# Kernel tuning notes

Hardware: AMD Instinct MI355X
Metric: run time of the kernel (lower is better)

## Reference

```python
import jax, jax.numpy as jnp
import numpy as np

N_HEADS = 8; N_LEVELS = 4; T_WINDOW = 2; N_CURR = 4; N_TEMP = 2; D_MODEL = 256
D_HEAD = D_MODEL // N_HEADS
SHAPES = [[4, 32, 48], [4, 16, 24], [4, 8, 12], [4, 4, 6]]  # (T, H, W) per level
LEN_IN = sum(t * h * w for t, h, w in SHAPES)  # 8160
LEN_Q = LEN_IN
N_BATCH = 1


def _bilinear_sample(value_l, loc):
    # value_l: (N, M, H, W, D); loc: (N, M, Q, P, 2) normalized to [0, 1].
    # Matches torch grid_sample(mode='bilinear', padding_mode='zeros', align_corners=False)
    # with grid = 2*loc - 1, i.e. pixel coords x = loc_x*W - 0.5, y = loc_y*H - 0.5.
    N, M, H, W, D = value_l.shape
    Q, P = loc.shape[2], loc.shape[3]
    x = loc[..., 0] * W - 0.5
    y = loc[..., 1] * H - 0.5
    x0 = jnp.floor(x); y0 = jnp.floor(y)
    wx = x - x0; wy = y - y0
    flat = value_l.reshape(N, M, H * W, D)

    def gather(xi, yi):
        valid = ((xi >= 0) & (xi < W) & (yi >= 0) & (yi < H)).astype(value_l.dtype)
        idx = (jnp.clip(yi, 0, H - 1) * W + jnp.clip(xi, 0, W - 1)).astype(jnp.int32)
        g = jnp.take_along_axis(flat, idx.reshape(N, M, Q * P, 1), axis=2)
        return g.reshape(N, M, Q, P, D) * valid[..., None]

    v00 = gather(x0, y0); v10 = gather(x0 + 1.0, y0)
    v01 = gather(x0, y0 + 1.0); v11 = gather(x0 + 1.0, y0 + 1.0)
    return (v00 * ((1 - wx) * (1 - wy))[..., None] + v10 * (wx * (1 - wy))[..., None]
            + v01 * ((1 - wx) * wy)[..., None] + v11 * (wx * wy)[..., None])


def _forward(query, reference_points, temporal_offsets, input_flatten, shapes, starts,
             Wv, bv, Ws, bs, Wa, ba, Wts, bts, Wta, bta, Wo, bo):
    N, Lq, _ = query.shape
    value = (input_flatten @ Wv + bv).reshape(N, -1, N_HEADS, D_HEAD)
    ts_off = (query @ Wts + bts).reshape(N, Lq, N_HEADS, N_LEVELS, T_WINDOW, N_TEMP, 2)
    t_attn = (query @ Wta + bta).reshape(N, Lq, N_HEADS, N_LEVELS * T_WINDOW * N_TEMP)
    c_attn = (query @ Wa + ba).reshape(N, Lq, N_HEADS, N_LEVELS * N_CURR)
    # joint softmax over current + temporal sampling points (as in the source)
    attn = jax.nn.softmax(jnp.concatenate([c_attn, t_attn], axis=-1), axis=-1)
    aw_c = attn[..., :N_LEVELS * N_CURR].reshape(N, Lq, N_HEADS, N_LEVELS, N_CURR)
    aw_t = attn[..., N_LEVELS * N_CURR:].reshape(N, Lq, N_HEADS, N_LEVELS, T_WINDOW * N_TEMP)
    aw = jnp.concatenate([aw_c, aw_t], axis=4)  # (N, Lq, M, L, P)
    c_off = (query @ Ws + bs).reshape(N, Lq, N_HEADS, N_LEVELS, N_CURR, 2)
    # flattened-temporal grid per level: width W_l, height T_l*H_l
    norm = jnp.array([[w, t * h] for t, h, w in shapes], dtype=query.dtype)  # (L, 2)
    loc_c = reference_points[:, :, None, :, None, :] + c_off / norm[None, None, None, :, None, :]
    loc_t = (reference_points[:, :, None, :, None, None, :]
             + temporal_offsets[:, :, None, :, :, None, :]
             + ts_off / norm[None, None, None, :, None, None, :])
    loc_t = loc_t.reshape(N, Lq, N_HEADS, N_LEVELS, T_WINDOW * N_TEMP, 2)
    locs = jnp.concatenate([loc_c, loc_t], axis=4)  # (N, Lq, M, L, P, 2)
    out = jnp.zeros((N, N_HEADS, Lq, D_HEAD), query.dtype)
    for l, (t, h, w) in enumerate(shapes):
        s = starts[l]
        vl = value[:, s:s + t * h * w].transpose(0, 2, 1, 3).reshape(N, N_HEADS, t * h, w, D_HEAD)
        loc_l = locs[:, :, :, l].transpose(0, 2, 1, 3, 4)   # (N, M, Lq, P, 2)
        sampled = _bilinear_sample(vl, loc_l)               # (N, M, Lq, P, Dh)
        w_l = aw[:, :, :, l].transpose(0, 2, 1, 3)          # (N, M, Lq, P)
        out = out + jnp.einsum('nmqpd,nmqp->nmqd', sampled, w_l)
    out = out.transpose(0, 2, 1, 3).reshape(N, Lq, D_MODEL)
    return out @ Wo + bo


def setup_inputs() -> dict:
    key = jax.random.key(0)
    ks = jax.random.split(key, 18)
    D = D_MODEL
    sc = 0.02
    query = jax.random.normal(ks[0], (N_BATCH, LEN_Q, D), jnp.float32)
    reference_points = jax.random.uniform(ks[1], (N_BATCH, LEN_Q, N_LEVELS, 2), jnp.float32)
    temporal_offsets = jax.random.uniform(ks[2], (N_BATCH, LEN_Q, N_LEVELS, T_WINDOW, 2),
                                          jnp.float32, minval=-0.25, maxval=0.25)
    input_flatten = jax.random.normal(ks[3], (N_BATCH, LEN_IN, D), jnp.float32)
    input_spatial_shapes = jnp.array(SHAPES, dtype=jnp.int32)
    starts = np.cumsum([0] + [t * h * w for t, h, w in SHAPES])[:-1]
    input_level_start_index = jnp.array(starts, dtype=jnp.int32)
    n_off = N_HEADS * N_LEVELS * N_CURR * 2          # 256
    n_att = N_HEADS * N_LEVELS * N_CURR              # 128
    n_toff = N_HEADS * N_LEVELS * T_WINDOW * N_TEMP * 2  # 256
    n_tatt = N_HEADS * N_LEVELS * T_WINDOW * N_TEMP      # 128
    return {
        'query': query, 'reference_points': reference_points,
        'temporal_offsets': temporal_offsets, 'input_flatten': input_flatten,
        'input_spatial_shapes': input_spatial_shapes,
        'input_level_start_index': input_level_start_index,
        'Wv': jax.random.normal(ks[4], (D, D), jnp.float32) * sc,
        'bv': jnp.zeros((D,), jnp.float32),
        'Ws': jax.random.normal(ks[5], (D, n_off), jnp.float32) * sc,
        'bs': jax.random.normal(ks[6], (n_off,), jnp.float32) * 2.0,
        'Wa': jax.random.normal(ks[7], (D, n_att), jnp.float32) * sc,
        'ba': jnp.zeros((n_att,), jnp.float32),
        'Wts': jax.random.normal(ks[8], (D, n_toff), jnp.float32) * sc,
        'bts': jax.random.normal(ks[9], (n_toff,), jnp.float32) * 2.0,
        'Wta': jax.random.normal(ks[10], (D, n_tatt), jnp.float32) * sc,
        'bta': jnp.zeros((n_tatt,), jnp.float32),
        'Wo': jax.random.normal(ks[11], (D, D), jnp.float32) * sc,
        'bo': jnp.zeros((D,), jnp.float32),
    }


def reference(query, reference_points, temporal_offsets, input_flatten,
              input_spatial_shapes, input_level_start_index,
              Wv, bv, Ws, bs, Wa, ba, Wts, bts, Wta, bta, Wo, bo):
    shapes = [tuple(int(v) for v in row) for row in np.asarray(input_spatial_shapes)]
    starts = [int(v) for v in np.asarray(input_level_start_index)]
    return _forward(query, reference_points, temporal_offsets, input_flatten,
                    shapes, starts, Wv, bv, Ws, bs, Wa, ba, Wts, bts, Wta, bta, Wo, bo)
```

## Files before the change

kernel.cpp:

```cpp
#include <hip/hip_runtime.h>


#define LEN 8160
#define NPACK8 (1280 * 256 / 8)

typedef __attribute__((ext_vector_type(8))) short bf16x8;
typedef __attribute__((ext_vector_type(8))) unsigned short u16x8;
typedef __attribute__((ext_vector_type(4))) float f32x4;

__device__ __forceinline__ unsigned short rne_bf16(float v)
{
    unsigned u = __float_as_uint(v);
    return (unsigned short)((u + 0x7FFFu + ((u >> 16) & 1u)) >> 16);
}

__device__ __forceinline__ void split_bf16(float v, unsigned short* hi, unsigned short* lo)
{
    unsigned u = __float_as_uint(v);
    unsigned r = (u + 0x7FFFu + ((u >> 16) & 1u)) & 0xFFFF0000u;
    float hif = __uint_as_float(r);
    float lof = v - hif;
    unsigned ul = __float_as_uint(lof);
    unsigned rl = (ul + 0x7FFFu + ((ul >> 16) & 1u)) >> 16;
    *hi = (unsigned short)(r >> 16);
    *lo = (unsigned short)rl;
}

__device__ __forceinline__ float bf2f(unsigned short s)
{
    return __uint_as_float(((unsigned)s) << 16);
}

__device__ __forceinline__ void splitA8(const float* a, bf16x8* hi, bf16x8* lo)
{
    float4 x = *(const float4*)a;
    float4 y = *(const float4*)(a + 4);
    unsigned short h[8], l[8];
    split_bf16(x.x, &h[0], &l[0]); split_bf16(x.y, &h[1], &l[1]);
    split_bf16(x.z, &h[2], &l[2]); split_bf16(x.w, &h[3], &l[3]);
    split_bf16(y.x, &h[4], &l[4]); split_bf16(y.y, &h[5], &l[5]);
    split_bf16(y.z, &h[6], &l[6]); split_bf16(y.w, &h[7], &l[7]);
    bf16x8 hv, lv;
    #pragma unroll
    for (int i = 0; i < 8; i++) { hv[i] = (short)h[i]; lv[i] = (short)l[i]; }
    *hi = hv; *lo = lv;
}

__global__ __launch_bounds__(256) void prep_kernel(
    const float* __restrict__ Ws, const float* __restrict__ bs,
    const float* __restrict__ Wa, const float* __restrict__ ba,
    const float* __restrict__ Wts, const float* __restrict__ bts,
    const float* __restrict__ Wta, const float* __restrict__ bta,
    const float* __restrict__ Wv, const float* __restrict__ Wo,
    unsigned short* __restrict__ Whi, unsigned short* __restrict__ Wlo,
    float* __restrict__ bcat)
{
    int idx = blockIdx.x * 256 + threadIdx.x;
    if (idx < NPACK8) {
        int n = idx >> 5;
        int k0 = (idx & 31) << 3;
        unsigned short h[8], l[8];
        #pragma unroll
        for (int t = 0; t < 8; t++) {
            int k = k0 + t;
            float v;
            if (n < 256) v = Wv[k * 256 + n];
            else if (n < 1024) {
                int j = n - 256;
                if (j < 256)      v = Ws [k * 256 + j];
                else if (j < 384) v = Wa [k * 128 + (j - 256)];
                else if (j < 640) v = Wts[k * 256 + (j - 384)];
                else              v = Wta[k * 128 + (j - 640)];
            } else v = Wo[k * 256 + (n - 1024)];
            split_bf16(v, &h[t], &l[t]);
        }
        uint4 hv, lv;
        hv.x = h[0] | ((unsigned)h[1] << 16); hv.y = h[2] | ((unsigned)h[3] << 16);
        hv.z = h[4] | ((unsigned)h[5] << 16); hv.w = h[6] | ((unsigned)h[7] << 16);
        lv.x = l[0] | ((unsigned)l[1] << 16); lv.y = l[2] | ((unsigned)l[3] << 16);
        lv.z = l[4] | ((unsigned)l[5] << 16); lv.w = l[6] | ((unsigned)l[7] << 16);
        *(uint4*)(Whi + n * 256 + k0) = hv;
        *(uint4*)(Wlo + n * 256 + k0) = lv;
    } else if (idx < NPACK8 + 768) {
        int j = idx - NPACK8;
        float v;
        if (j < 256)      v = bs[j];
        else if (j < 384) v = ba[j - 256];
        else if (j < 640) v = bts[j - 384];
        else              v = bta[j - 640];
        bcat[j] = v;
    }
}

__global__ __launch_bounds__(256) void gemm_mfma_dual(
    const float* __restrict__ A0,
    const unsigned short* __restrict__ B0hi, const unsigned short* __restrict__ B0lo,
    const float* __restrict__ bias0, void* __restrict__ C0, int N0, int mode0, int nbx0,
    const float* __restrict__ A1,
    const unsigned short* __restrict__ B1hi, const unsigned short* __restrict__ B1lo,
    const float* __restrict__ bias1, void* __restrict__ C1, int N1, int mode1)
{
    __shared__ unsigned short Bf[2 * 4 * 4 * 64 * 8];
    const int tid = threadIdx.x;
    const int wave = tid >> 6, lane = tid & 63;
    int bx = blockIdx.x;
    const int by = blockIdx.y;

    const float* A;
    const unsigned short *Bhi, *Blo;
    const float* bias; void* C; int N, mode;
    if (bx < nbx0) {
        A = A0; Bhi = B0hi; Blo = B0lo;
        bias = bias0; C = C0; N = N0; mode = mode0;
    } else {
        bx -= nbx0;
        A = A1; Bhi = B1hi; Blo = B1lo;
        bias = bias1; C = C1; N = N1; mode = mode1;
    }

    const int lm = lane & 15;
    const int kq = lane >> 4;
    const int m0 = by * 128 + wave * 32 + lm;
    const int ra = min(m0, LEN - 1);
    const int rb = min(m0 + 16, LEN - 1);
    const float* aP0 = A + (size_t)ra * 256 + kq * 8;
    const float* aP1 = A + (size_t)rb * 256 + kq * 8;

    f32x4 acc[2][4] = {};
    #pragma unroll
    for (int chunk = 0; chunk < 2; chunk++) {
        #pragma unroll
        for (int t = 0; t < 8; t++) {
            int f = t * 256 + tid;
            int ln = f & 63, nt = (f >> 6) & 3, kt = (f >> 8) & 3, pl = f >> 10;
            const unsigned short* src = (pl ? Blo : Bhi)
                + (size_t)(bx * 64 + nt * 16 + (ln & 15)) * 256
                + chunk * 128 + kt * 32 + (ln >> 4) * 8;
            *(uint4*)(&Bf[(size_t)f * 8]) = *(const uint4*)src;
        }
        __syncthreads();
        #pragma unroll
        for (int kt = 0; kt < 4; kt++) {
            const int ko = chunk * 128 + kt * 32;
            bf16x8 ah0, al0, ah1, al1;
            splitA8(aP0 + ko, &ah0, &al0);
            splitA8(aP1 + ko, &ah1, &al1);
            #pragma unroll
            for (int nt = 0; nt < 4; nt++) {
                const int fb = (kt * 4 + nt) * 64 + lane;
                bf16x8 bh = *(const bf16x8*)(&Bf[(size_t)fb * 8]);
                bf16x8 bl = *(const bf16x8*)(&Bf[(size_t)(fb + 1024) * 8]);
                acc[0][nt] = __builtin_amdgcn_mfma_f32_16x16x32_bf16(ah0, bh, acc[0][nt], 0, 0, 0);
                acc[0][nt] = __builtin_amdgcn_mfma_f32_16x16x32_bf16(ah0, bl, acc[0][nt], 0, 0, 0);
                acc[0][nt] = __builtin_amdgcn_mfma_f32_16x16x32_bf16(al0, bh, acc[0][nt], 0, 0, 0);
                acc[1][nt] = __builtin_amdgcn_mfma_f32_16x16x32_bf16(ah1, bh, acc[1][nt], 0, 0, 0);
                acc[1][nt] = __builtin_amdgcn_mfma_f32_16x16x32_bf16(ah1, bl, acc[1][nt], 0, 0, 0);
                acc[1][nt] = __builtin_amdgcn_mfma_f32_16x16x32_bf16(al1, bh, acc[1][nt], 0, 0, 0);
            }
        }
        __syncthreads();
    }

    const int col = bx * 64 + lm;
    #pragma unroll
    for (int sub = 0; sub < 2; sub++) {
        const int row0 = by * 128 + wave * 32 + sub * 16 + kq * 4;
        #pragma unroll
        for (int nt = 0; nt < 4; nt++) {
            int c = col + nt * 16;
            float bb = bias[c];
            #pragma unroll
            for (int r = 0; r < 4; r++) {
                int row = row0 + r;
                if (row < LEN) {
                    float v = acc[sub][nt][r] + bb;
                    if (mode) {
                        ((unsigned short*)C)[(size_t)(c >> 5) * 8192 * 32
                                             + (size_t)row * 32 + (c & 31)] = rne_bf16(v);
                    } else {
                        ((float*)C)[(size_t)row * N + c] = v;
                    }
                }
            }
        }
    }
}

__global__ __launch_bounds__(256) void sample_kernel(
    const unsigned short* __restrict__ value,
    const float* __restrict__ proj,
    const float* __restrict__ refp,
    const float* __restrict__ toff,
    float* __restrict__ attn)
{
    const int q = blockIdx.x;
    const int head = threadIdx.x >> 5;
    const int lane = threadIdx.x & 31;
    __shared__ int2   s_row[8][32];
    __shared__ float4 s_w[8][32];

    const float* p = proj + (size_t)q * 768;

    {
        const int i = lane;
        float logit, ox, oy, rx, ry;
        int l;
        if (i < 16) {
            l = i >> 2; int pt2 = i & 3;
            logit = p[256 + head * 16 + i];
            ox = p[head * 32 + l * 8 + pt2 * 2 + 0];
            oy = p[head * 32 + l * 8 + pt2 * 2 + 1];
            rx = refp[q * 8 + l * 2 + 0];
            ry = refp[q * 8 + l * 2 + 1];
        } else {
            int j = i - 16; l = j >> 2;
            int tp = j & 3, tw = tp >> 1, nt = tp & 1;
            logit = p[640 + head * 16 + j];
            ox = p[384 + head * 32 + l * 8 + tw * 4 + nt * 2 + 0];
            oy = p[384 + head * 32 + l * 8 + tw * 4 + nt * 2 + 1];
            rx = refp[q * 8 + l * 2 + 0] + toff[q * 16 + l * 4 + tw * 2 + 0];
            ry = refp[q * 8 + l * 2 + 1] + toff[q * 16 + l * 4 + tw * 2 + 1];
        }
        const int Wl = 48 >> l;
        const int Hgl = 128 >> l;
        const int st = 8192 - (8192 >> (2 * l));
        const float fW = (float)Wl, fHg = (float)Hgl;
        float x = (rx + ox / fW) * fW - 0.5f;
        float y = (ry + oy / fHg) * fHg - 0.5f;

        float mx = logit;
        #pragma unroll
        for (int off = 16; off > 0; off >>= 1)
            mx = fmaxf(mx, __shfl_xor(mx, off, 32));
        float e = expf(logit - mx);
        float s = e;
        #pragma unroll
        for (int off = 16; off > 0; off >>= 1)
            s += __shfl_xor(s, off, 32);
        float w = e / s;

        float fx = floorf(x), fy = floorf(y);
        float wx = x - fx, wy = y - fy;
        int x0 = (int)fx, y0 = (int)fy;
        int x1 = x0 + 1, y1 = y0 + 1;
        float mx0 = ((unsigned)x0 < (unsigned)Wl) ? 1.f : 0.f;
        float mx1 = ((unsigned)x1 < (unsigned)Wl) ? 1.f : 0.f;
        float my0 = ((unsigned)y0 < (unsigned)Hgl) ? 1.f : 0.f;
        float my1 = ((unsigned)y1 < (unsigned)Hgl) ? 1.f : 0.f;
        int cx0 = min(max(x0, 0), Wl - 1), cx1 = min(max(x1, 0), Wl - 1);
        int cy0 = min(max(y0, 0), Hgl - 1), cy1 = min(max(y1, 0), Hgl - 1);
        int xb = min(max(x0, 0), Wl - 2);
        float sx0 = 1.f - wx, sy0 = 1.f - wy;
        float aL = (cx0 == xb     ? sx0 * mx0 : 0.f) + (cx1 == xb     ? wx * mx1 : 0.f);
        float aR = (cx0 == xb + 1 ? sx0 * mx0 : 0.f) + (cx1 == xb + 1 ? wx * mx1 : 0.f);
        float by0 = sy0 * my0, by1 = wy * my1;
        int2 rr;
        rr.x = (st + cy0 * Wl + xb) * 64;
        rr.y = (st + cy1 * Wl + xb) * 64;
        float4 ww;
        ww.x = w * aL * by0;
        ww.y = w * aR * by0;
        ww.z = w * aL * by1;
        ww.w = w * aR * by1;
        s_row[head][lane] = rr;
        s_w[head][lane] = ww;
    }
    __syncthreads();

    const int pt4  = lane >> 3;
    const int half = (lane >> 2) & 1;
    const int cg   = lane & 3;
    const char* vbase = (const char*)value + head * (8192 * 64) + half * 64 + cg * 16;
    float acc[8] = {0.f, 0.f, 0.f, 0.f, 0.f, 0.f, 0.f, 0.f};
    #pragma unroll
    for (int i = 0; i < 8; i++) {
        int pidx = (i << 2) | pt4;
        int2 rr = s_row[head][pidx];
        float4 ww = s_w[head][pidx];
        u16x8 v0 = *(const u16x8*)(vbase + rr.x);
        u16x8 v1 = *(const u16x8*)(vbase + rr.y);
        float w0 = half ? ww.y : ww.x;
        float w1 = half ? ww.w : ww.z;
        #pragma unroll
        for (int j = 0; j < 8; j++) {
            acc[j] = fmaf(w0, bf2f(v0[j]), acc[j]);
            acc[j] = fmaf(w1, bf2f(v1[j]), acc[j]);
        }
    }
    #pragma unroll
    for (int off = 4; off <= 16; off <<= 1)
        #pragma unroll
        for (int j = 0; j < 8; j++)
            acc[j] += __shfl_xor(acc[j], off, 32);

    if (lane < 4) {
        size_t o = (size_t)q * 256 + head * 32 + cg * 8;
        *(float4*)(attn + o)     = make_float4(acc[0], acc[1], acc[2], acc[3]);
        *(float4*)(attn + o + 4) = make_float4(acc[4], acc[5], acc[6], acc[7]);
    }
}

extern "C" void kernel_launch(void* const* d_in, const int* in_sizes, int n_in,
                              void* d_out, int out_size, void* d_ws, size_t ws_size,
                              hipStream_t stream)
{
    const float* query = (const float*)d_in[0];
    const float* refp  = (const float*)d_in[1];
    const float* toff  = (const float*)d_in[2];
    const float* inpf  = (const float*)d_in[3];
    const float* Wv  = (const float*)d_in[6];
    const float* bv  = (const float*)d_in[7];
    const float* Ws_ = (const float*)d_in[8];
    const float* bs_ = (const float*)d_in[9];
    const float* Wa  = (const float*)d_in[10];
    const float* ba  = (const float*)d_in[11];
    const float* Wts = (const float*)d_in[12];
    const float* bts = (const float*)d_in[13];
    const float* Wta = (const float*)d_in[14];
    const float* bta = (const float*)d_in[15];
    const float* Wo  = (const float*)d_in[16];
    const float* bo  = (const float*)d_in[17];
    float* out = (float*)d_out;

    unsigned short* value_bf = (unsigned short*)d_ws;
    float* proj = (float*)(value_bf + (size_t)8 * 8192 * 32);
    float* attn = proj + (size_t)LEN * 768;
    unsigned short* Whi = (unsigned short*)(attn + (size_t)LEN * 256);
    unsigned short* Wlo = Whi + 1280 * 256;
    float* bcat = (float*)(Wlo + 1280 * 256);

    prep_kernel<<<164, 256, 0, stream>>>(Ws_, bs_, Wa, ba, Wts, bts, Wta, bta,
                                         Wv, Wo, Whi, Wlo, bcat);
    gemm_mfma_dual<<<dim3(16, 64), 256, 0, stream>>>(
        inpf, Whi, Wlo, bv, value_bf, 256, 1, 4,
        query, Whi + 256 * 256, Wlo + 256 * 256, bcat, proj, 768, 0);
    sample_kernel<<<LEN, 256, 0, stream>>>(value_bf, proj, refp, toff, attn);
    gemm_mfma_dual<<<dim3(4, 64), 256, 0, stream>>>(
        attn, Whi + 1024 * 256, Wlo + 1024 * 256, bo, out, 256, 0, 4,
        attn, Whi + 1024 * 256, Wlo + 1024 * 256, bo, out, 256, 0);
}
```

Before: 174.9 us.

## Pre-split attention output to bf16 hi/lo, use direct-to-LDS B loads, halve output GEMM tile

The sampling kernel now writes its result as separate bf16 hi and lo planes, so the output projection GEMM loads pre-split A operands instead of splitting fp32 on the fly. The GEMM is templated on rows per wave and A format, and the output projection runs with 64-row tiles over twice as many blocks to raise occupancy. B-tile staging switches to global_load_lds direct-to-LDS transfers with an explicit vmcnt wait. This adds split work to the sampler's epilogue and changes the LDS layout of the staged B tiles.

```diff
diff --git a/kernel.cpp b/kernel.cpp
--- a/kernel.cpp
+++ b/kernel.cpp
@@ -3,6 +3,9 @@
 
 #define LEN 8160
 #define NPACK8 (1280 * 256 / 8)
+
+#define AS1 __attribute__((address_space(1)))
+#define AS3 __attribute__((address_space(3)))
 
 typedef __attribute__((ext_vector_type(8))) short bf16x8;
 typedef __attribute__((ext_vector_type(8))) unsigned short u16x8;
@@ -92,6 +95,7 @@
     }
 }
 
+template <int MSUB, int AFMT>
 __global__ __launch_bounds__(256) void gemm_mfma_dual(
     const float* __restrict__ A0,
     const unsigned short* __restrict__ B0hi, const unsigned short* __restrict__ B0lo,
@@ -100,7 +104,7 @@
     const unsigned short* __restrict__ B1hi, const unsigned short* __restrict__ B1lo,
     const float* __restrict__ bias1, void* __restrict__ C1, int N1, int mode1)
 {
-    __shared__ unsigned short Bf[2 * 4 * 4 * 64 * 8];
+    __shared__ __align__(16) unsigned short Bf[2 * 4 * 4 * 64 * 8];
     const int tid = threadIdx.x;
     const int wave = tid >> 6, lane = tid & 63;
     int bx = blockIdx.x;
@@ -120,31 +124,59 @@
 
     const int lm = lane & 15;
     const int kq = lane >> 4;
-    const int m0 = by * 128 + wave * 32 + lm;
+    const int m0 = by * (MSUB * 64) + wave * (MSUB * 16) + lm;
     const int ra = min(m0, LEN - 1);
     const int rb = min(m0 + 16, LEN - 1);
+
     const float* aP0 = A + (size_t)ra * 256 + kq * 8;
     const float* aP1 = A + (size_t)rb * 256 + kq * 8;
-
-    f32x4 acc[2][4] = {};
+    const unsigned short* Ah = (const unsigned short*)A;
+    const unsigned short* ahP0 = Ah + (size_t)ra * 256 + kq * 8;
+    const unsigned short* alP0 = Ah + (size_t)LEN * 256 + (size_t)ra * 256 + kq * 8;
+    const unsigned short* ahP1 = Ah + (size_t)rb * 256 + kq * 8;
+    const unsigned short* alP1 = Ah + (size_t)LEN * 256 + (size_t)rb * 256 + kq * 8;
+
+    f32x4 acc[MSUB][4] = {};
     #pragma unroll
     for (int chunk = 0; chunk < 2; chunk++) {
         #pragma unroll
         for (int t = 0; t < 8; t++) {
-            int f = t * 256 + tid;
-            int ln = f & 63, nt = (f >> 6) & 3, kt = (f >> 8) & 3, pl = f >> 10;
+            const int g  = t * 4 + wave;
+            const int nt = g & 3, kt = (g >> 2) & 3, pl = g >> 4;
             const unsigned short* src = (pl ? Blo : Bhi)
-                + (size_t)(bx * 64 + nt * 16 + (ln & 15)) * 256
-                + chunk * 128 + kt * 32 + (ln >> 4) * 8;
-            *(uint4*)(&Bf[(size_t)f * 8]) = *(const uint4*)src;
-        }
+                + (size_t)(bx * 64 + nt * 16 + (lane & 15)) * 256
+                + chunk * 128 + kt * 32 + (lane >> 4) * 8;
+            __builtin_amdgcn_global_load_lds(
+                (AS1 void*)(uintptr_t)src,
+                (AS3 void*)&Bf[(size_t)g * 64 * 8],
+                16, 0, 0);
+        }
+        bf16x8 pah[MSUB][4], pal[MSUB][4];
+        if constexpr (AFMT == 1) {
+            #pragma unroll
+            for (int kt = 0; kt < 4; kt++) {
+                const int ko = chunk * 128 + kt * 32;
+                pah[0][kt] = *(const bf16x8*)(ahP0 + ko);
+                pal[0][kt] = *(const bf16x8*)(alP0 + ko);
+                if constexpr (MSUB == 2) {
+                    pah[1][kt] = *(const bf16x8*)(ahP1 + ko);
+                    pal[1][kt] = *(const bf16x8*)(alP1 + ko);
+                }
+            }
+        }
+        asm volatile("s_waitcnt vmcnt(0)" ::: "memory");
         __syncthreads();
         #pragma unroll
         for (int kt = 0; kt < 4; kt++) {
             const int ko = chunk * 128 + kt * 32;
             bf16x8 ah0, al0, ah1, al1;
-            splitA8(aP0 + ko, &ah0, &al0);
-            splitA8(aP1 + ko, &ah1, &al1);
+            if constexpr (AFMT == 0) {
+                splitA8(aP0 + ko, &ah0, &al0);
+                if constexpr (MSUB == 2) splitA8(aP1 + ko, &ah1, &al1);
+            } else {
+                ah0 = pah[0][kt]; al0 = pal[0][kt];
+                if constexpr (MSUB == 2) { ah1 = pah[1][kt]; al1 = pal[1][kt]; }
+            }
             #pragma unroll
             for (int nt = 0; nt < 4; nt++) {
                 const int fb = (kt * 4 + nt) * 64 + lane;
@@ -153,9 +185,11 @@
                 acc[0][nt] = __builtin_amdgcn_mfma_f32_16x16x32_bf16(ah0, bh, acc[0][nt], 0, 0, 0);
                 acc[0][nt] = __builtin_amdgcn_mfma_f32_16x16x32_bf16(ah0, bl, acc[0][nt], 0, 0, 0);
                 acc[0][nt] = __builtin_amdgcn_mfma_f32_16x16x32_bf16(al0, bh, acc[0][nt], 0, 0, 0);
-                acc[1][nt] = __builtin_amdgcn_mfma_f32_16x16x32_bf16(ah1, bh, acc[1][nt], 0, 0, 0);
-                acc[1][nt] = __builtin_amdgcn_mfma_f32_16x16x32_bf16(ah1, bl, acc[1][nt], 0, 0, 0);
-                acc[1][nt] = __builtin_amdgcn_mfma_f32_16x16x32_bf16(al1, bh, acc[1][nt], 0, 0, 0);
+                if constexpr (MSUB == 2) {
+                    acc[1][nt] = __builtin_amdgcn_mfma_f32_16x16x32_bf16(ah1, bh, acc[1][nt], 0, 0, 0);
+                    acc[1][nt] = __builtin_amdgcn_mfma_f32_16x16x32_bf16(ah1, bl, acc[1][nt], 0, 0, 0);
+                    acc[1][nt] = __builtin_amdgcn_mfma_f32_16x16x32_bf16(al1, bh, acc[1][nt], 0, 0, 0);
+                }
             }
         }
         __syncthreads();
@@ -163,8 +197,8 @@
 
     const int col = bx * 64 + lm;
     #pragma unroll
-    for (int sub = 0; sub < 2; sub++) {
-        const int row0 = by * 128 + wave * 32 + sub * 16 + kq * 4;
+    for (int sub = 0; sub < MSUB; sub++) {
+        const int row0 = by * (MSUB * 64) + wave * (MSUB * 16) + sub * 16 + kq * 4;
         #pragma unroll
         for (int nt = 0; nt < 4; nt++) {
             int c = col + nt * 16;
@@ -191,7 +225,7 @@
     const float* __restrict__ proj,
     const float* __restrict__ refp,
     const float* __restrict__ toff,
-    float* __restrict__ attn)
+    unsigned short* __restrict__ attn)
 {
     const int q = blockIdx.x;
     const int head = threadIdx.x >> 5;
@@ -295,8 +329,16 @@
 
     if (lane < 4) {
         size_t o = (size_t)q * 256 + head * 32 + cg * 8;
-        *(float4*)(attn + o)     = make_float4(acc[0], acc[1], acc[2], acc[3]);
-        *(float4*)(attn + o + 4) = make_float4(acc[4], acc[5], acc[6], acc[7]);
+        unsigned short h[8], l[8];
+        #pragma unroll
+        for (int j = 0; j < 8; j++) split_bf16(acc[j], &h[j], &l[j]);
+        uint4 hv, lv;
+        hv.x = h[0] | ((unsigned)h[1] << 16); hv.y = h[2] | ((unsigned)h[3] << 16);
+        hv.z = h[4] | ((unsigned)h[5] << 16); hv.w = h[6] | ((unsigned)h[7] << 16);
+        lv.x = l[0] | ((unsigned)l[1] << 16); lv.y = l[2] | ((unsigned)l[3] << 16);
+        lv.z = l[4] | ((unsigned)l[5] << 16); lv.w = l[6] | ((unsigned)l[7] << 16);
+        *(uint4*)(attn + o) = hv;
+        *(uint4*)(attn + (size_t)LEN * 256 + o) = lv;
     }
 }
 
@@ -324,18 +366,18 @@
 
     unsigned short* value_bf = (unsigned short*)d_ws;
     float* proj = (float*)(value_bf + (size_t)8 * 8192 * 32);
-    float* attn = proj + (size_t)LEN * 768;
-    unsigned short* Whi = (unsigned short*)(attn + (size_t)LEN * 256);
+    unsigned short* attn_hl = (unsigned short*)(proj + (size_t)LEN * 768);
+    unsigned short* Whi = attn_hl + (size_t)2 * LEN * 256;
     unsigned short* Wlo = Whi + 1280 * 256;
     float* bcat = (float*)(Wlo + 1280 * 256);
 
     prep_kernel<<<164, 256, 0, stream>>>(Ws_, bs_, Wa, ba, Wts, bts, Wta, bta,
                                          Wv, Wo, Whi, Wlo, bcat);
-    gemm_mfma_dual<<<dim3(16, 64), 256, 0, stream>>>(
+    gemm_mfma_dual<2, 0><<<dim3(16, 64), 256, 0, stream>>>(
         inpf, Whi, Wlo, bv, value_bf, 256, 1, 4,
         query, Whi + 256 * 256, Wlo + 256 * 256, bcat, proj, 768, 0);
-    sample_kernel<<<LEN, 256, 0, stream>>>(value_bf, proj, refp, toff, attn);
-    gemm_mfma_dual<<<dim3(4, 64), 256, 0, stream>>>(
-        attn, Whi + 1024 * 256, Wlo + 1024 * 256, bo, out, 256, 0, 4,
-        attn, Whi + 1024 * 256, Wlo + 1024 * 256, bo, out, 256, 0);
-}
+    sample_kernel<<<LEN, 256, 0, stream>>>(value_bf, proj, refp, toff, attn_hl);
+    gemm_mfma_dual<1, 1><<<dim3(4, 128), 256, 0, stream>>>(
+        (const float*)attn_hl, Whi + 1024 * 256, Wlo + 1024 * 256, bo, out, 256, 0, 4,
+        (const float*)attn_hl, Whi + 1024 * 256, Wlo + 1024 * 256, bo, out, 256, 0);
+}
```

Result: no change. 172.9 us (-1.1%).

## Fuse deformable sampling with output projection and use direct global-to-LDS loads

Applied to the files above, without the earlier changes.

The sampling kernel now handles 16 queries per 512-thread block, two teams of eight queries each. It keeps the sampled attention rows in shared memory and runs the output projection GEMM (split-bf16 MFMA) in place, so the attn buffer no longer goes through global memory and one launch is dropped. The GEMM B-tile staging now uses global_load_lds to write straight into LDS instead of going through registers. The trade-offs are a much smaller grid (510 blocks), per-query serial loops inside each team, and Wo tiles read straight from global memory by every block.

```diff
diff --git a/kernel.cpp b/kernel.cpp
--- a/kernel.cpp
+++ b/kernel.cpp
@@ -3,6 +3,9 @@
 
 #define LEN 8160
 #define NPACK8 (1280 * 256 / 8)
+
+#define AS1 __attribute__((address_space(1)))
+#define AS3 __attribute__((address_space(3)))
 
 typedef __attribute__((ext_vector_type(8))) short bf16x8;
 typedef __attribute__((ext_vector_type(8))) unsigned short u16x8;
@@ -100,7 +103,7 @@
     const unsigned short* __restrict__ B1hi, const unsigned short* __restrict__ B1lo,
     const float* __restrict__ bias1, void* __restrict__ C1, int N1, int mode1)
 {
-    __shared__ unsigned short Bf[2 * 4 * 4 * 64 * 8];
+    __shared__ __align__(16) unsigned short Bf[2 * 4 * 4 * 64 * 8];
     const int tid = threadIdx.x;
     const int wave = tid >> 6, lane = tid & 63;
     int bx = blockIdx.x;
@@ -131,13 +134,17 @@
     for (int chunk = 0; chunk < 2; chunk++) {
         #pragma unroll
         for (int t = 0; t < 8; t++) {
-            int f = t * 256 + tid;
-            int ln = f & 63, nt = (f >> 6) & 3, kt = (f >> 8) & 3, pl = f >> 10;
+            const int g  = t * 4 + wave;
+            const int nt = g & 3, kt = (g >> 2) & 3, pl = g >> 4;
             const unsigned short* src = (pl ? Blo : Bhi)
-                + (size_t)(bx * 64 + nt * 16 + (ln & 15)) * 256
-                + chunk * 128 + kt * 32 + (ln >> 4) * 8;
-            *(uint4*)(&Bf[(size_t)f * 8]) = *(const uint4*)src;
-        }
+                + (size_t)(bx * 64 + nt * 16 + (lane & 15)) * 256
+                + chunk * 128 + kt * 32 + (lane >> 4) * 8;
+            __builtin_amdgcn_global_load_lds(
+                (AS1 void*)(uintptr_t)src,
+                (AS3 void*)&Bf[(size_t)g * 64 * 8],
+                16, 0, 0);
+        }
+        asm volatile("s_waitcnt vmcnt(0)" ::: "memory");
         __syncthreads();
         #pragma unroll
         for (int kt = 0; kt < 4; kt++) {
@@ -186,117 +193,157 @@
     }
 }
 
-__global__ __launch_bounds__(256) void sample_kernel(
+__global__ __launch_bounds__(512, 4) void fused_sample_out(
     const unsigned short* __restrict__ value,
     const float* __restrict__ proj,
     const float* __restrict__ refp,
     const float* __restrict__ toff,
-    float* __restrict__ attn)
-{
-    const int q = blockIdx.x;
-    const int head = threadIdx.x >> 5;
+    const unsigned short* __restrict__ WoThi,
+    const unsigned short* __restrict__ WoTlo,
+    const float* __restrict__ bo,
+    float* __restrict__ out)
+{
+    const int team = threadIdx.x >> 8;
+    const int head = (threadIdx.x >> 5) & 7;
     const int lane = threadIdx.x & 31;
-    __shared__ int2   s_row[8][32];
-    __shared__ float4 s_w[8][32];
-
-    const float* p = proj + (size_t)q * 768;
-
-    {
-        const int i = lane;
-        float logit, ox, oy, rx, ry;
-        int l;
-        if (i < 16) {
-            l = i >> 2; int pt2 = i & 3;
-            logit = p[256 + head * 16 + i];
-            ox = p[head * 32 + l * 8 + pt2 * 2 + 0];
-            oy = p[head * 32 + l * 8 + pt2 * 2 + 1];
-            rx = refp[q * 8 + l * 2 + 0];
-            ry = refp[q * 8 + l * 2 + 1];
-        } else {
-            int j = i - 16; l = j >> 2;
-            int tp = j & 3, tw = tp >> 1, nt = tp & 1;
-            logit = p[640 + head * 16 + j];
-            ox = p[384 + head * 32 + l * 8 + tw * 4 + nt * 2 + 0];
-            oy = p[384 + head * 32 + l * 8 + tw * 4 + nt * 2 + 1];
-            rx = refp[q * 8 + l * 2 + 0] + toff[q * 16 + l * 4 + tw * 2 + 0];
-            ry = refp[q * 8 + l * 2 + 1] + toff[q * 16 + l * 4 + tw * 2 + 1];
-        }
-        const int Wl = 48 >> l;
-        const int Hgl = 128 >> l;
-        const int st = 8192 - (8192 >> (2 * l));
-        const float fW = (float)Wl, fHg = (float)Hgl;
-        float x = (rx + ox / fW) * fW - 0.5f;
-        float y = (ry + oy / fHg) * fHg - 0.5f;
-
-        float mx = logit;
-        #pragma unroll
-        for (int off = 16; off > 0; off >>= 1)
-            mx = fmaxf(mx, __shfl_xor(mx, off, 32));
-        float e = expf(logit - mx);
-        float s = e;
-        #pragma unroll
-        for (int off = 16; off > 0; off >>= 1)
-            s += __shfl_xor(s, off, 32);
-        float w = e / s;
-
-        float fx = floorf(x), fy = floorf(y);
-        float wx = x - fx, wy = y - fy;
-        int x0 = (int)fx, y0 = (int)fy;
-        int x1 = x0 + 1, y1 = y0 + 1;
-        float mx0 = ((unsigned)x0 < (unsigned)Wl) ? 1.f : 0.f;
-        float mx1 = ((unsigned)x1 < (unsigned)Wl) ? 1.f : 0.f;
-        float my0 = ((unsigned)y0 < (unsigned)Hgl) ? 1.f : 0.f;
-        float my1 = ((unsigned)y1 < (unsigned)Hgl) ? 1.f : 0.f;
-        int cx0 = min(max(x0, 0), Wl - 1), cx1 = min(max(x1, 0), Wl - 1);
-        int cy0 = min(max(y0, 0), Hgl - 1), cy1 = min(max(y1, 0), Hgl - 1);
-        int xb = min(max(x0, 0), Wl - 2);
-        float sx0 = 1.f - wx, sy0 = 1.f - wy;
-        float aL = (cx0 == xb     ? sx0 * mx0 : 0.f) + (cx1 == xb     ? wx * mx1 : 0.f);
-        float aR = (cx0 == xb + 1 ? sx0 * mx0 : 0.f) + (cx1 == xb + 1 ? wx * mx1 : 0.f);
-        float by0 = sy0 * my0, by1 = wy * my1;
-        int2 rr;
-        rr.x = (st + cy0 * Wl + xb) * 64;
-        rr.y = (st + cy1 * Wl + xb) * 64;
-        float4 ww;
-        ww.x = w * aL * by0;
-        ww.y = w * aR * by0;
-        ww.z = w * aL * by1;
-        ww.w = w * aR * by1;
-        s_row[head][lane] = rr;
-        s_w[head][lane] = ww;
-    }
-    __syncthreads();
+    const int q0 = blockIdx.x * 16;
+
+    __shared__ int2   s_row[2][8][32];
+    __shared__ float4 s_w[2][8][32];
+    __shared__ float  attn_s[16][260];
 
     const int pt4  = lane >> 3;
     const int half = (lane >> 2) & 1;
     const int cg   = lane & 3;
     const char* vbase = (const char*)value + head * (8192 * 64) + half * 64 + cg * 16;
-    float acc[8] = {0.f, 0.f, 0.f, 0.f, 0.f, 0.f, 0.f, 0.f};
-    #pragma unroll
-    for (int i = 0; i < 8; i++) {
-        int pidx = (i << 2) | pt4;
-        int2 rr = s_row[head][pidx];
-        float4 ww = s_w[head][pidx];
-        u16x8 v0 = *(const u16x8*)(vbase + rr.x);
-        u16x8 v1 = *(const u16x8*)(vbase + rr.y);
-        float w0 = half ? ww.y : ww.x;
-        float w1 = half ? ww.w : ww.z;
-        #pragma unroll
-        for (int j = 0; j < 8; j++) {
-            acc[j] = fmaf(w0, bf2f(v0[j]), acc[j]);
-            acc[j] = fmaf(w1, bf2f(v1[j]), acc[j]);
-        }
-    }
-    #pragma unroll
-    for (int off = 4; off <= 16; off <<= 1)
-        #pragma unroll
-        for (int j = 0; j < 8; j++)
-            acc[j] += __shfl_xor(acc[j], off, 32);
-
-    if (lane < 4) {
-        size_t o = (size_t)q * 256 + head * 32 + cg * 8;
-        *(float4*)(attn + o)     = make_float4(acc[0], acc[1], acc[2], acc[3]);
-        *(float4*)(attn + o + 4) = make_float4(acc[4], acc[5], acc[6], acc[7]);
+
+    for (int qi = 0; qi < 8; qi++) {
+        const int q = q0 + team * 8 + qi;
+        const float* p = proj + (size_t)q * 768;
+
+        {
+            const int i = lane;
+            float logit, ox, oy, rx, ry;
+            int l;
+            if (i < 16) {
+                l = i >> 2; int pt2 = i & 3;
+                logit = p[256 + head * 16 + i];
+                ox = p[head * 32 + l * 8 + pt2 * 2 + 0];
+                oy = p[head * 32 + l * 8 + pt2 * 2 + 1];
+                rx = refp[q * 8 + l * 2 + 0];
+                ry = refp[q * 8 + l * 2 + 1];
+            } else {
+                int j = i - 16; l = j >> 2;
+                int tp = j & 3, tw = tp >> 1, nt = tp & 1;
+                logit = p[640 + head * 16 + j];
+                ox = p[384 + head * 32 + l * 8 + tw * 4 + nt * 2 + 0];
+                oy = p[384 + head * 32 + l * 8 + tw * 4 + nt * 2 + 1];
+                rx = refp[q * 8 + l * 2 + 0] + toff[q * 16 + l * 4 + tw * 2 + 0];
+                ry = refp[q * 8 + l * 2 + 1] + toff[q * 16 + l * 4 + tw * 2 + 1];
+            }
+            const int Wl = 48 >> l;
+            const int Hgl = 128 >> l;
+            const int st = 8192 - (8192 >> (2 * l));
+            const float fW = (float)Wl, fHg = (float)Hgl;
+            float x = (rx + ox / fW) * fW - 0.5f;
+            float y = (ry + oy / fHg) * fHg - 0.5f;
+
+            float mx = logit;
+            #pragma unroll
+            for (int off = 16; off > 0; off >>= 1)
+                mx = fmaxf(mx, __shfl_xor(mx, off, 32));
+            float e = expf(logit - mx);
+            float s = e;
+            #pragma unroll
+            for (int off = 16; off > 0; off >>= 1)
+                s += __shfl_xor(s, off, 32);
+            float w = e / s;
+
+            float fx = floorf(x), fy = floorf(y);
+            float wx = x - fx, wy = y - fy;
+            int x0 = (int)fx, y0 = (int)fy;
+            int x1 = x0 + 1, y1 = y0 + 1;
+            float mx0 = ((unsigned)x0 < (unsigned)Wl) ? 1.f : 0.f;
+            float mx1 = ((unsigned)x1 < (unsigned)Wl) ? 1.f : 0.f;
+            float my0 = ((unsigned)y0 < (unsigned)Hgl) ? 1.f : 0.f;
+            float my1 = ((unsigned)y1 < (unsigned)Hgl) ? 1.f : 0.f;
+            int cx0 = min(max(x0, 0), Wl - 1), cx1 = min(max(x1, 0), Wl - 1);
+            int cy0 = min(max(y0, 0), Hgl - 1), cy1 = min(max(y1, 0), Hgl - 1);
+            int xb = min(max(x0, 0), Wl - 2);
+            float sx0 = 1.f - wx, sy0 = 1.f - wy;
+            float aL = (cx0 == xb     ? sx0 * mx0 : 0.f) + (cx1 == xb     ? wx * mx1 : 0.f);
+            float aR = (cx0 == xb + 1 ? sx0 * mx0 : 0.f) + (cx1 == xb + 1 ? wx * mx1 : 0.f);
+            float by0 = sy0 * my0, by1 = wy * my1;
+            int2 rr;
+            rr.x = (st + cy0 * Wl + xb) * 64;
+            rr.y = (st + cy1 * Wl + xb) * 64;
+            float4 ww;
+            ww.x = w * aL * by0;
+            ww.y = w * aR * by0;
+            ww.z = w * aL * by1;
+            ww.w = w * aR * by1;
+            s_row[team][head][lane] = rr;
+            s_w[team][head][lane] = ww;
+        }
+
+        float acc[8] = {0.f, 0.f, 0.f, 0.f, 0.f, 0.f, 0.f, 0.f};
+        #pragma unroll
+        for (int i = 0; i < 8; i++) {
+            int pidx = (i << 2) | pt4;
+            int2 rr = s_row[team][head][pidx];
+            float4 ww = s_w[team][head][pidx];
+            u16x8 v0 = *(const u16x8*)(vbase + rr.x);
+            u16x8 v1 = *(const u16x8*)(vbase + rr.y);
+            float w0 = half ? ww.y : ww.x;
+            float w1 = half ? ww.w : ww.z;
+            #pragma unroll
+            for (int j = 0; j < 8; j++) {
+                acc[j] = fmaf(w0, bf2f(v0[j]), acc[j]);
+                acc[j] = fmaf(w1, bf2f(v1[j]), acc[j]);
+            }
+        }
+        #pragma unroll
+        for (int off = 4; off <= 16; off <<= 1)
+            #pragma unroll
+            for (int j = 0; j < 8; j++)
+                acc[j] += __shfl_xor(acc[j], off, 32);
+
+        if (lane < 4) {
+            float* dst = &attn_s[team * 8 + qi][head * 32 + cg * 8];
+            *(float4*)dst       = make_float4(acc[0], acc[1], acc[2], acc[3]);
+            *(float4*)(dst + 4) = make_float4(acc[4], acc[5], acc[6], acc[7]);
+        }
+    }
+    __syncthreads();
+
+    const int wv = threadIdx.x >> 6;
+    const int l  = threadIdx.x & 63;
+    const int lm = l & 15, kq = l >> 4;
+    f32x4 acc2[2] = {};
+    #pragma unroll
+    for (int ks = 0; ks < 8; ks++) {
+        bf16x8 ah, al;
+        splitA8(&attn_s[lm][ks * 32 + kq * 8], &ah, &al);
+        #pragma unroll
+        for (int nt = 0; nt < 2; nt++) {
+            const int col = wv * 32 + nt * 16 + lm;
+            const size_t bofs = (size_t)col * 256 + ks * 32 + kq * 8;
+            bf16x8 bh = *(const bf16x8*)(WoThi + bofs);
+            bf16x8 bl = *(const bf16x8*)(WoTlo + bofs);
+            acc2[nt] = __builtin_amdgcn_mfma_f32_16x16x32_bf16(ah, bh, acc2[nt], 0, 0, 0);
+            acc2[nt] = __builtin_amdgcn_mfma_f32_16x16x32_bf16(ah, bl, acc2[nt], 0, 0, 0);
+            acc2[nt] = __builtin_amdgcn_mfma_f32_16x16x32_bf16(al, bh, acc2[nt], 0, 0, 0);
+        }
+    }
+    #pragma unroll
+    for (int nt = 0; nt < 2; nt++) {
+        const int col = wv * 32 + nt * 16 + lm;
+        const float bb = bo[col];
+        #pragma unroll
+        for (int r = 0; r < 4; r++) {
+            const int row = kq * 4 + r;
+            out[(size_t)(q0 + row) * 256 + col] = acc2[nt][r] + bb;
+        }
     }
 }
 
@@ -324,8 +371,7 @@
 
     unsigned short* value_bf = (unsigned short*)d_ws;
     float* proj = (float*)(value_bf + (size_t)8 * 8192 * 32);
-    float* attn = proj + (size_t)LEN * 768;
-    unsigned short* Whi = (unsigned short*)(attn + (size_t)LEN * 256);
+    unsigned short* Whi = (unsigned short*)(proj + (size_t)LEN * 768);
     unsigned short* Wlo = Whi + 1280 * 256;
     float* bcat = (float*)(Wlo + 1280 * 256);
 
@@ -334,8 +380,7 @@
     gemm_mfma_dual<<<dim3(16, 64), 256, 0, stream>>>(
         inpf, Whi, Wlo, bv, value_bf, 256, 1, 4,
         query, Whi + 256 * 256, Wlo + 256 * 256, bcat, proj, 768, 0);
-    sample_kernel<<<LEN, 256, 0, stream>>>(value_bf, proj, refp, toff, attn);
-    gemm_mfma_dual<<<dim3(4, 64), 256, 0, stream>>>(
-        attn, Whi + 1024 * 256, Wlo + 1024 * 256, bo, out, 256, 0, 4,
-        attn, Whi + 1024 * 256, Wlo + 1024 * 256, bo, out, 256, 0);
-}
+    fused_sample_out<<<510, 512, 0, stream>>>(
+        value_bf, proj, refp, toff,
+        Whi + 1024 * 256, Wlo + 1024 * 256, bo, out);
+}
```

Result: slower. 180.2 us (+3.1%).
